# Optimization experiments

Measured on AMD Instinct MI355X. Metric: run time of the kernel, lower is better.

Reference implementation:

```python
import jax, jax.numpy as jnp
import numpy as np

N, F_IN, E = 16384, 512, 524288
H1, H2 = 32, 16


def gcn_conv(x, src, dst, W, b, n):
    # PyG GCNConv: linear (no bias) -> symmetric-normalized neighbor sum
    # (self-loops already appended to src/dst) -> add bias.
    deg = jnp.zeros((n,), x.dtype).at[dst].add(jnp.ones((src.shape[0],), x.dtype))
    dinv = jax.lax.rsqrt(deg)  # deg >= 1 thanks to self-loops
    norm = dinv[src] * dinv[dst]  # [E+N]
    xw = x @ W                    # [N, out]
    msg = xw[src] * norm[:, None] # gather over edges
    out = jnp.zeros((n, W.shape[1]), x.dtype).at[dst].add(msg)  # scatter-add
    return out + b


def setup_inputs() -> dict:
    key = jax.random.key(0)
    ks = jax.random.split(key, 8)
    x = jax.random.normal(ks[0], (N, F_IN), jnp.float32)
    edge_index = jax.random.randint(ks[1], (2, E), 0, N, jnp.int64)
    def glorot(k, shp):
        lim = np.sqrt(6.0 / (shp[0] + shp[1])).astype(np.float32)
        return jax.random.uniform(k, shp, jnp.float32, -lim, lim)
    return {
        "x": x,
        "edge_index": edge_index,
        "W1": glorot(ks[2], (F_IN, H1)), "b1": jnp.zeros((H1,), jnp.float32),
        "W2": glorot(ks[3], (H1, H2)),  "b2": jnp.zeros((H2,), jnp.float32),
        "W3": glorot(ks[4], (H1, H2)),  "b3": jnp.zeros((H2,), jnp.float32),
        "num_nodes": N,
    }


def reference(x, edge_index, W1, b1, W2, b2, W3, b3, num_nodes):
    n = num_nodes
    loops = jnp.arange(n, dtype=edge_index.dtype)
    src = jnp.concatenate([edge_index[0], loops])
    dst = jnp.concatenate([edge_index[1], loops])
    h1 = gcn_conv(x, src, dst, W1, b1, n)
    mu = gcn_conv(h1, src, dst, W2, b2, n)
    logvar = gcn_conv(h1, src, dst, W3, b3, n)
    z = mu  # eval mode: reparameterize returns mu, decoder dropout is a no-op
    adj = jax.nn.sigmoid(z @ z.T)  # [N, N] inner-product decode
    return adj, mu, logvar
```

## Files before the change

### kernel.cpp

```cpp
#include <hip/hip_runtime.h>
#include <hip/hip_bf16.h>

#define N_NODES 16384
#define F_IN    512
#define N_EDGE  524288
#define H1      32
#define H2      16

typedef float f32x4 __attribute__((ext_vector_type(4)));

#define OFF_CNT     0u
#define OFF_ROWPTR  16448u
#define OFF_CURSOR  32896u
#define OFF_SRCS    49344u
#define OFF_DINV    573632u
#define OFF_XW1     590080u
#define OFF_XW2     1114368u
#define OFF_XW3     1376512u

__device__ __forceinline__ float sigf(float x) {
    float e = __expf(-x);
    return __builtin_amdgcn_rcpf(1.0f + e);
}

__global__ __launch_bounds__(256) void hist_k(const int* __restrict__ ei,
                                              unsigned* __restrict__ cnt) {
    int e = blockIdx.x * 256 + threadIdx.x;
    atomicAdd(&cnt[ei[N_EDGE + e]], 1u);
}

__global__ __launch_bounds__(1024) void scan_k(const unsigned* __restrict__ cnt,
                                               unsigned* __restrict__ rowptr,
                                               unsigned* __restrict__ cursor,
                                               float* __restrict__ dinv) {
    const int t = threadIdx.x;
    unsigned vals[16];
    const uint4* c4 = (const uint4*)cnt;
#pragma unroll
    for (int i = 0; i < 4; ++i) {
        uint4 v = c4[t * 4 + i];
        vals[i * 4 + 0] = v.x; vals[i * 4 + 1] = v.y;
        vals[i * 4 + 2] = v.z; vals[i * 4 + 3] = v.w;
    }
    unsigned loc[16], s = 0;
#pragma unroll
    for (int i = 0; i < 16; ++i) { loc[i] = s; s += vals[i]; }

    const int lane = t & 63, w = t >> 6;
    unsigned v = s;
#pragma unroll
    for (int off = 1; off < 64; off <<= 1) {
        unsigned u = __shfl_up(v, off);
        if (lane >= off) v += u;
    }
    __shared__ unsigned wtot[16];
    if (lane == 63) wtot[w] = v;
    __syncthreads();
    if (t == 0) {
        unsigned run = 0;
#pragma unroll
        for (int i = 0; i < 16; ++i) { unsigned x = wtot[i]; wtot[i] = run; run += x; }
        rowptr[N_NODES] = run;
    }
    __syncthreads();
    unsigned base = wtot[w] + v - s;
#pragma unroll
    for (int i = 0; i < 16; ++i) {
        unsigned rp = base + loc[i];
        rowptr[t * 16 + i] = rp;
        cursor[t * 16 + i] = rp;
        dinv[t * 16 + i] = rsqrtf((float)(vals[i] + 1u));
    }
}

__global__ __launch_bounds__(256) void fill_k(const int* __restrict__ ei,
                                              unsigned* __restrict__ cursor,
                                              int* __restrict__ srcs) {
    int e = blockIdx.x * 256 + threadIdx.x;
    int d = ei[N_EDGE + e];
    unsigned p = atomicAdd(&cursor[d], 1u);
    srcs[p] = ei[e];
}

__global__ __launch_bounds__(256) void gemm1_k(const float* __restrict__ x,
                                               const float* __restrict__ W,
                                               float* __restrict__ xw) {
    int tid = blockIdx.x * 256 + threadIdx.x;
    int row = tid >> 3, cq = tid & 7;
    const float4* x4 = (const float4*)(x + (size_t)row * F_IN);
    const float4* W4 = (const float4*)W;
    float ax = 0.f, ay = 0.f, az = 0.f, aw = 0.f;
#pragma unroll 4
    for (int k4 = 0; k4 < F_IN / 4; ++k4) {
        float4 xv = x4[k4];
        float4 w0 = W4[(size_t)(4 * k4 + 0) * 8 + cq];
        float4 w1 = W4[(size_t)(4 * k4 + 1) * 8 + cq];
        float4 w2 = W4[(size_t)(4 * k4 + 2) * 8 + cq];
        float4 w3 = W4[(size_t)(4 * k4 + 3) * 8 + cq];
        ax = fmaf(xv.x, w0.x, ax); ay = fmaf(xv.x, w0.y, ay);
        az = fmaf(xv.x, w0.z, az); aw = fmaf(xv.x, w0.w, aw);
        ax = fmaf(xv.y, w1.x, ax); ay = fmaf(xv.y, w1.y, ay);
        az = fmaf(xv.y, w1.z, az); aw = fmaf(xv.y, w1.w, aw);
        ax = fmaf(xv.z, w2.x, ax); ay = fmaf(xv.z, w2.y, ay);
        az = fmaf(xv.z, w2.z, az); aw = fmaf(xv.z, w2.w, aw);
        ax = fmaf(xv.w, w3.x, ax); ay = fmaf(xv.w, w3.y, ay);
        az = fmaf(xv.w, w3.z, az); aw = fmaf(xv.w, w3.w, aw);
    }
    float4 o; o.x = ax; o.y = ay; o.z = az; o.w = aw;
    ((float4*)xw)[(size_t)row * 8 + cq] = o;
}

__global__ __launch_bounds__(256) void conv1_k(const float* __restrict__ xw1,
                                               const float* __restrict__ dinv,
                                               const int* __restrict__ srcs,
                                               const unsigned* __restrict__ rowptr,
                                               const float* __restrict__ b1,
                                               const float* __restrict__ W2,
                                               const float* __restrict__ W3,
                                               float* __restrict__ xw2,
                                               float* __restrict__ xw3) {
    const int t = threadIdx.x;
    const int node = blockIdx.x * 8 + (t >> 5);
    const int c = t & 31;
    unsigned e0 = rowptr[node], e1 = rowptr[node + 1];
    float sum = 0.f;
    for (unsigned e = e0; e < e1; ++e) {
        int s = srcs[e];
        sum = fmaf(xw1[(size_t)s * H1 + c], dinv[s], sum);
    }
    float di = dinv[node];
    float h = fmaf(di, sum, di * di * xw1[(size_t)node * H1 + c]) + b1[c];
    __shared__ float h1s[8][H1 + 1];
    h1s[t >> 5][c] = h;
    __syncthreads();
    const float* Wm = (c < H2) ? W2 : W3;
    int q = c & (H2 - 1);
    float acc = 0.f;
#pragma unroll
    for (int k = 0; k < H1; ++k) acc = fmaf(h1s[t >> 5][k], Wm[k * H2 + q], acc);
    if (c < H2) xw2[(size_t)node * H2 + q] = acc;
    else        xw3[(size_t)node * H2 + q] = acc;
}

__global__ __launch_bounds__(256) void conv2_k(const float* __restrict__ xw2,
                                               const float* __restrict__ xw3,
                                               const float* __restrict__ dinv,
                                               const int* __restrict__ srcs,
                                               const unsigned* __restrict__ rowptr,
                                               const float* __restrict__ b2,
                                               const float* __restrict__ b3,
                                               float* __restrict__ out_mu,
                                               float* __restrict__ out_lv) {
    const int t = threadIdx.x;
    const int node = blockIdx.x * 8 + (t >> 5);
    const int c = t & 31;
    const int q = c & (H2 - 1);
    const float* feat = (c < H2) ? xw2 : xw3;
    unsigned e0 = rowptr[node], e1 = rowptr[node + 1];
    float sum = 0.f;
    for (unsigned e = e0; e < e1; ++e) {
        int s = srcs[e];
        sum = fmaf(feat[(size_t)s * H2 + q], dinv[s], sum);
    }
    float di = dinv[node];
    float v = fmaf(di, sum, di * di * feat[(size_t)node * H2 + q]) +
              ((c < H2) ? b2[q] : b3[q]);
    if (c < H2) out_mu[(size_t)node * H2 + q] = v;
    else        out_lv[(size_t)node * H2 + q] = v;
}

__global__ __launch_bounds__(256) void adj_k(const float* __restrict__ z,
                                             float* __restrict__ out) {
    __shared__ float4 zr[512];
    __shared__ float4 zc[512];
    const int t = threadIdx.x;
    const int row0 = blockIdx.y << 7, col0 = blockIdx.x << 7;
    const float4* z4 = (const float4*)z;
#pragma unroll
    for (int i = 0; i < 2; ++i) {
        int idx = t + i * 256;
        int r = idx >> 2, kk = idx & 3;
        int sw = (kk ^ (r >> 3)) & 3;
        zr[(r << 2) + sw] = z4[(size_t)(row0 + r) * 4 + kk];
        zc[(r << 2) + sw] = z4[(size_t)(col0 + r) * 4 + kk];
    }
    __syncthreads();
    const int cg = t & 15, rg = t >> 4;
    float acc[8][8];
#pragma unroll
    for (int r = 0; r < 8; ++r)
#pragma unroll
        for (int c = 0; c < 8; ++c) acc[r][c] = 0.f;

#pragma unroll
    for (int kk = 0; kk < 4; ++kk) {
        float4 a[8], b[8];
#pragma unroll
        for (int r = 0; r < 8; ++r) a[r] = zr[((rg * 8 + r) << 2) + ((kk ^ rg) & 3)];
#pragma unroll
        for (int j = 0; j < 4; ++j) {
            int cA = cg * 4 + j, cB = 64 + cg * 4 + j;
            b[j]     = zc[(cA << 2) + ((kk ^ (cA >> 3)) & 3)];
            b[4 + j] = zc[(cB << 2) + ((kk ^ (cB >> 3)) & 3)];
        }
#pragma unroll
        for (int r = 0; r < 8; ++r)
#pragma unroll
            for (int c = 0; c < 8; ++c) {
                acc[r][c] = fmaf(a[r].x, b[c].x, acc[r][c]);
                acc[r][c] = fmaf(a[r].y, b[c].y, acc[r][c]);
                acc[r][c] = fmaf(a[r].z, b[c].z, acc[r][c]);
                acc[r][c] = fmaf(a[r].w, b[c].w, acc[r][c]);
            }
    }
#pragma unroll
    for (int r = 0; r < 8; ++r) {
        int row = row0 + rg * 8 + r;
        f32x4 o0, o1;
        o0.x = sigf(acc[r][0]); o0.y = sigf(acc[r][1]);
        o0.z = sigf(acc[r][2]); o0.w = sigf(acc[r][3]);
        o1.x = sigf(acc[r][4]); o1.y = sigf(acc[r][5]);
        o1.z = sigf(acc[r][6]); o1.w = sigf(acc[r][7]);
        float* base = out + (size_t)row * N_NODES + col0;
        __builtin_nontemporal_store(o0, (f32x4*)(base + cg * 4));
        __builtin_nontemporal_store(o1, (f32x4*)(base + 64 + cg * 4));
    }
}

extern "C" void kernel_launch(void* const* d_in, const int* in_sizes, int n_in,
                              void* d_out, int out_size, void* d_ws, size_t ws_size,
                              hipStream_t stream) {
    const float* x  = (const float*)d_in[0];
    const int*   ei = (const int*)d_in[1];
    const float* W1 = (const float*)d_in[2];
    const float* b1 = (const float*)d_in[3];
    const float* W2 = (const float*)d_in[4];
    const float* b2 = (const float*)d_in[5];
    const float* W3 = (const float*)d_in[6];
    const float* b3 = (const float*)d_in[7];
    float* out = (float*)d_out;

    unsigned* ws   = (unsigned*)d_ws;
    unsigned* cnt    = ws + OFF_CNT;
    unsigned* rowptr = ws + OFF_ROWPTR;
    unsigned* cursor = ws + OFF_CURSOR;
    int*      srcs   = (int*)(ws + OFF_SRCS);
    float*    dinv   = (float*)(ws + OFF_DINV);
    float*    xw1    = (float*)(ws + OFF_XW1);
    float*    xw2    = (float*)(ws + OFF_XW2);
    float*    xw3    = (float*)(ws + OFF_XW3);

    float* out_mu = out + (size_t)N_NODES * N_NODES;
    float* out_lv = out_mu + (size_t)N_NODES * H2;

    (void)hipMemsetAsync(cnt, 0, N_NODES * sizeof(unsigned), stream);
    hist_k<<<N_EDGE / 256, 256, 0, stream>>>(ei, cnt);
    scan_k<<<1, 1024, 0, stream>>>(cnt, rowptr, cursor, dinv);
    fill_k<<<N_EDGE / 256, 256, 0, stream>>>(ei, cursor, srcs);
    gemm1_k<<<(N_NODES * 8) / 256, 256, 0, stream>>>(x, W1, xw1);
    conv1_k<<<N_NODES / 8, 256, 0, stream>>>(xw1, dinv, srcs, rowptr, b1, W2, W3, xw2, xw3);
    conv2_k<<<N_NODES / 8, 256, 0, stream>>>(xw2, xw3, dinv, srcs, rowptr, b2, b3, out_mu, out_lv);
    adj_k<<<dim3(N_NODES / 128, N_NODES / 128), 256, 0, stream>>>(out_mu, out);
}
```

Before: 341.9 us.

## Persistent row-strip adj tiles with register prefetch; interleave xw2/xw3 buffers

The decoder kernel now launches 2048 blocks. Each block keeps its 128-row z tile in LDS and walks 8 consecutive 128-column tiles, prefetching the next column tile into registers while it computes and stores the current one. This cuts launch and block count and overlaps global loads with compute, at the cost of serialising eight tiles per block and adding barriers. Separately, the mu and logvar projected features are stored interleaved in one 32-wide buffer, so each gather in conv2 reads one contiguous 128-byte row instead of two 64-byte halves.

```diff
diff --git a/kernel.cpp b/kernel.cpp
--- a/kernel.cpp
+++ b/kernel.cpp
@@ -15,12 +15,17 @@
 #define OFF_SRCS    49344u
 #define OFF_DINV    573632u
 #define OFF_XW1     590080u
-#define OFF_XW2     1114368u
-#define OFF_XW3     1376512u
+#define OFF_XW23    1114368u
 
 __device__ __forceinline__ float sigf(float x) {
     float e = __expf(-x);
     return __builtin_amdgcn_rcpf(1.0f + e);
+}
+
+__device__ __forceinline__ void sync_lds() {
+    asm volatile("s_waitcnt lgkmcnt(0)" ::: "memory");
+    __builtin_amdgcn_s_barrier();
+    asm volatile("" ::: "memory");
 }
 
 __global__ __launch_bounds__(256) void hist_k(const int* __restrict__ ei,
@@ -117,8 +122,7 @@
                                                const float* __restrict__ b1,
                                                const float* __restrict__ W2,
                                                const float* __restrict__ W3,
-                                               float* __restrict__ xw2,
-                                               float* __restrict__ xw3) {
+                                               float* __restrict__ xw23) {
     const int t = threadIdx.x;
     const int node = blockIdx.x * 8 + (t >> 5);
     const int c = t & 31;
@@ -138,12 +142,10 @@
     float acc = 0.f;
 #pragma unroll
     for (int k = 0; k < H1; ++k) acc = fmaf(h1s[t >> 5][k], Wm[k * H2 + q], acc);
-    if (c < H2) xw2[(size_t)node * H2 + q] = acc;
-    else        xw3[(size_t)node * H2 + q] = acc;
-}
-
-__global__ __launch_bounds__(256) void conv2_k(const float* __restrict__ xw2,
-                                               const float* __restrict__ xw3,
+    xw23[(size_t)node * 32 + c] = acc;
+}
+
+__global__ __launch_bounds__(256) void conv2_k(const float* __restrict__ xw23,
                                                const float* __restrict__ dinv,
                                                const int* __restrict__ srcs,
                                                const unsigned* __restrict__ rowptr,
@@ -155,15 +157,14 @@
     const int node = blockIdx.x * 8 + (t >> 5);
     const int c = t & 31;
     const int q = c & (H2 - 1);
-    const float* feat = (c < H2) ? xw2 : xw3;
     unsigned e0 = rowptr[node], e1 = rowptr[node + 1];
     float sum = 0.f;
     for (unsigned e = e0; e < e1; ++e) {
         int s = srcs[e];
-        sum = fmaf(feat[(size_t)s * H2 + q], dinv[s], sum);
+        sum = fmaf(xw23[(size_t)s * 32 + c], dinv[s], sum);
     }
     float di = dinv[node];
-    float v = fmaf(di, sum, di * di * feat[(size_t)node * H2 + q]) +
+    float v = fmaf(di, sum, di * di * xw23[(size_t)node * 32 + c]) +
               ((c < H2) ? b2[q] : b3[q]);
     if (c < H2) out_mu[(size_t)node * H2 + q] = v;
     else        out_lv[(size_t)node * H2 + q] = v;
@@ -174,56 +175,78 @@
     __shared__ float4 zr[512];
     __shared__ float4 zc[512];
     const int t = threadIdx.x;
-    const int row0 = blockIdx.y << 7, col0 = blockIdx.x << 7;
+    const int strip  = blockIdx.x >> 4;
+    const int cchunk = blockIdx.x & 15;
+    const int row0 = strip << 7;
     const float4* z4 = (const float4*)z;
-#pragma unroll
-    for (int i = 0; i < 2; ++i) {
-        int idx = t + i * 256;
-        int r = idx >> 2, kk = idx & 3;
-        int sw = (kk ^ (r >> 3)) & 3;
-        zr[(r << 2) + sw] = z4[(size_t)(row0 + r) * 4 + kk];
-        zc[(r << 2) + sw] = z4[(size_t)(col0 + r) * 4 + kk];
-    }
-    __syncthreads();
+
+    const int idx0 = t, idx1 = t + 256;
+    const int r0 = idx0 >> 2, k0 = idx0 & 3, s0 = (r0 << 2) + ((k0 ^ (r0 >> 3)) & 3);
+    const int r1 = idx1 >> 2, k1 = idx1 & 3, s1 = (r1 << 2) + ((k1 ^ (r1 >> 3)) & 3);
+
+    zr[s0] = z4[(size_t)(row0 + r0) * 4 + k0];
+    zr[s1] = z4[(size_t)(row0 + r1) * 4 + k1];
+
+    int col0 = (cchunk << 10);
+    float4 c0 = z4[(size_t)(col0 + r0) * 4 + k0];
+    float4 c1 = z4[(size_t)(col0 + r1) * 4 + k1];
+
     const int cg = t & 15, rg = t >> 4;
-    float acc[8][8];
-#pragma unroll
-    for (int r = 0; r < 8; ++r)
-#pragma unroll
-        for (int c = 0; c < 8; ++c) acc[r][c] = 0.f;
-
-#pragma unroll
-    for (int kk = 0; kk < 4; ++kk) {
-        float4 a[8], b[8];
-#pragma unroll
-        for (int r = 0; r < 8; ++r) a[r] = zr[((rg * 8 + r) << 2) + ((kk ^ rg) & 3)];
-#pragma unroll
-        for (int j = 0; j < 4; ++j) {
-            int cA = cg * 4 + j, cB = 64 + cg * 4 + j;
-            b[j]     = zc[(cA << 2) + ((kk ^ (cA >> 3)) & 3)];
-            b[4 + j] = zc[(cB << 2) + ((kk ^ (cB >> 3)) & 3)];
+
+    for (int tile = 0; tile < 8; ++tile) {
+        zc[s0] = c0;
+        zc[s1] = c1;
+        sync_lds();
+
+        if (tile < 7) {
+            int ncol0 = col0 + 128;
+            c0 = z4[(size_t)(ncol0 + r0) * 4 + k0];
+            c1 = z4[(size_t)(ncol0 + r1) * 4 + k1];
         }
+
+        float acc[8][8];
 #pragma unroll
         for (int r = 0; r < 8; ++r)
 #pragma unroll
-            for (int c = 0; c < 8; ++c) {
-                acc[r][c] = fmaf(a[r].x, b[c].x, acc[r][c]);
-                acc[r][c] = fmaf(a[r].y, b[c].y, acc[r][c]);
-                acc[r][c] = fmaf(a[r].z, b[c].z, acc[r][c]);
-                acc[r][c] = fmaf(a[r].w, b[c].w, acc[r][c]);
+            for (int c = 0; c < 8; ++c) acc[r][c] = 0.f;
+
+#pragma unroll
+        for (int kk = 0; kk < 4; ++kk) {
+            float4 a[8], b[8];
+#pragma unroll
+            for (int r = 0; r < 8; ++r) a[r] = zr[((rg * 8 + r) << 2) + ((kk ^ rg) & 3)];
+#pragma unroll
+            for (int j = 0; j < 4; ++j) {
+                int cA = cg * 4 + j, cB = 64 + cg * 4 + j;
+                b[j]     = zc[(cA << 2) + ((kk ^ (cA >> 3)) & 3)];
+                b[4 + j] = zc[(cB << 2) + ((kk ^ (cB >> 3)) & 3)];
             }
-    }
-#pragma unroll
-    for (int r = 0; r < 8; ++r) {
-        int row = row0 + rg * 8 + r;
-        f32x4 o0, o1;
-        o0.x = sigf(acc[r][0]); o0.y = sigf(acc[r][1]);
-        o0.z = sigf(acc[r][2]); o0.w = sigf(acc[r][3]);
-        o1.x = sigf(acc[r][4]); o1.y = sigf(acc[r][5]);
-        o1.z = sigf(acc[r][6]); o1.w = sigf(acc[r][7]);
-        float* base = out + (size_t)row * N_NODES + col0;
-        __builtin_nontemporal_store(o0, (f32x4*)(base + cg * 4));
-        __builtin_nontemporal_store(o1, (f32x4*)(base + 64 + cg * 4));
+#pragma unroll
+            for (int r = 0; r < 8; ++r)
+#pragma unroll
+                for (int c = 0; c < 8; ++c) {
+                    acc[r][c] = fmaf(a[r].x, b[c].x, acc[r][c]);
+                    acc[r][c] = fmaf(a[r].y, b[c].y, acc[r][c]);
+                    acc[r][c] = fmaf(a[r].z, b[c].z, acc[r][c]);
+                    acc[r][c] = fmaf(a[r].w, b[c].w, acc[r][c]);
+                }
+        }
+
+#pragma unroll
+        for (int r = 0; r < 8; ++r) {
+            int row = row0 + rg * 8 + r;
+            f32x4 o0, o1;
+            o0.x = sigf(acc[r][0]); o0.y = sigf(acc[r][1]);
+            o0.z = sigf(acc[r][2]); o0.w = sigf(acc[r][3]);
+            o1.x = sigf(acc[r][4]); o1.y = sigf(acc[r][5]);
+            o1.z = sigf(acc[r][6]); o1.w = sigf(acc[r][7]);
+            float* base = out + (size_t)row * N_NODES + col0;
+            __builtin_nontemporal_store(o0, (f32x4*)(base + cg * 4));
+            __builtin_nontemporal_store(o1, (f32x4*)(base + 64 + cg * 4));
+        }
+
+        sync_lds();
+        col0 += 128;
     }
 }
 
@@ -247,8 +270,7 @@
     int*      srcs   = (int*)(ws + OFF_SRCS);
     float*    dinv   = (float*)(ws + OFF_DINV);
     float*    xw1    = (float*)(ws + OFF_XW1);
-    float*    xw2    = (float*)(ws + OFF_XW2);
-    float*    xw3    = (float*)(ws + OFF_XW3);
+    float*    xw23   = (float*)(ws + OFF_XW23);
 
     float* out_mu = out + (size_t)N_NODES * N_NODES;
     float* out_lv = out_mu + (size_t)N_NODES * H2;
@@ -258,7 +280,7 @@
     scan_k<<<1, 1024, 0, stream>>>(cnt, rowptr, cursor, dinv);
     fill_k<<<N_EDGE / 256, 256, 0, stream>>>(ei, cursor, srcs);
     gemm1_k<<<(N_NODES * 8) / 256, 256, 0, stream>>>(x, W1, xw1);
-    conv1_k<<<N_NODES / 8, 256, 0, stream>>>(xw1, dinv, srcs, rowptr, b1, W2, W3, xw2, xw3);
-    conv2_k<<<N_NODES / 8, 256, 0, stream>>>(xw2, xw3, dinv, srcs, rowptr, b2, b3, out_mu, out_lv);
-    adj_k<<<dim3(N_NODES / 128, N_NODES / 128), 256, 0, stream>>>(out_mu, out);
-}
+    conv1_k<<<N_NODES / 8, 256, 0, stream>>>(xw1, dinv, srcs, rowptr, b1, W2, W3, xw23);
+    conv2_k<<<N_NODES / 8, 256, 0, stream>>>(xw23, dinv, srcs, rowptr, b2, b3, out_mu, out_lv);
+    adj_k<<<dim3(2048), 256, 0, stream>>>(out_mu, out);
+}
```

Measured after the change: 431.7 us. +26.3%, slower.
